# Kernel optimization log

Hardware: AMD Instinct MI355X
Metric: run time of the kernel (lower is better)

## Reference

```python
import jax, jax.numpy as jnp
import numpy as np

B, N, D, P, HMUL, K = 2, 4096, 64, 64, 4, 16
H = D * HMUL  # attn_mlp hidden = 256
EPS = 1e-5


def setup_inputs() -> dict:
    key = jax.random.key(0)
    ks = jax.random.split(key, 18)
    def lin(k, fan_in, shape):
        return (jax.random.normal(k, shape, dtype=jnp.float32) / np.sqrt(fan_in)).astype(jnp.float32)
    return {
        "x": jax.random.normal(ks[0], (B, N, D), dtype=jnp.float32),
        "pos": jax.random.uniform(ks[1], (B, N, 3), dtype=jnp.float32),
        "w_qkv": lin(ks[2], D, (D, 3 * D)), "b_qkv": jnp.zeros((3 * D,), jnp.float32),
        "w_p1": lin(ks[3], 3, (3, P)),     "b_p1": jnp.zeros((P,), jnp.float32),
        "w_p2": lin(ks[4], P, (P, D)),     "b_p2": jnp.zeros((D,), jnp.float32),
        "w_a1": lin(ks[5], D, (D, H)),     "b_a1": jnp.zeros((H,), jnp.float32),
        "w_a2": lin(ks[6], H, (H, D)),     "b_a2": jnp.zeros((D,), jnp.float32),
        "w_fc": lin(ks[7], D, (D, D)),     "b_fc": jnp.zeros((D,), jnp.float32),
        "gamma": jnp.ones((D,), jnp.float32), "beta": jnp.zeros((D,), jnp.float32),
    }


def reference(x, pos, w_qkv, b_qkv, w_p1, b_p1, w_p2, b_p2,
              w_a1, b_a1, w_a2, b_a2, w_fc, b_fc, gamma, beta):
    residual = x
    qkv = x @ w_qkv + b_qkv                      # [B,N,3D]
    q, k, v = jnp.split(qkv, 3, axis=-1)         # each [B,N,D]

    # full O(N^2) pairwise distances for KNN (smallest-k)
    rel = pos[:, :, None, :] - pos[:, None, :, :]       # [B,N,N,3]
    dist = jnp.sqrt(jnp.sum(rel * rel, axis=-1))        # [B,N,N]
    _, idx = jax.lax.top_k(-dist, K)                    # [B,N,K] nearest indices

    # gather neighbors (gather commutes with the pointwise MLPs the torch
    # code applies before its neighbor_select, so math is identical)
    gather = jax.vmap(lambda arr, i: arr[i])            # arr:[N,*], i:[N,K] -> [N,K,*]
    k_nb = gather(k, idx)                               # [B,N,K,D]
    v_nb = gather(v, idx)                               # [B,N,K,D]
    pos_nb = gather(pos, idx)                           # [B,N,K,3]

    qk_map = q[:, :, None, :] - k_nb                    # [B,N,K,D]
    rel_nb = pos[:, :, None, :] - pos_nb                # [B,N,K,3]
    pos_emb = jax.nn.relu(rel_nb @ w_p1 + b_p1) @ w_p2 + b_p2   # [B,N,K,D]

    h = qk_map + pos_emb
    scores = jax.nn.relu(h @ w_a1 + b_a1) @ w_a2 + b_a2          # [B,N,K,D]
    attn = jax.nn.softmax(scores, axis=-2)                       # over K neighbors
    agg = jnp.sum(attn * v_nb, axis=-2)                          # [B,N,D]

    agg = agg @ w_fc + b_fc
    # BatchNorm1d over channel dim D (training-mode batch stats over B and N)
    mean = jnp.mean(agg, axis=(0, 1))
    var = jnp.mean(jnp.square(agg - mean), axis=(0, 1))
    agg = (agg - mean) * jax.lax.rsqrt(var + EPS) * gamma + beta
    return jax.nn.relu(agg) + residual
```

## Files before the change

kernel.cpp:

```cpp
#include <hip/hip_runtime.h>
#include <hip/hip_bf16.h>
#include <math.h>

#define NPTS 4096
#define KNB 16
#define CAP 384
#define QPB 8

typedef __attribute__((ext_vector_type(8))) short bf16x8;
typedef __attribute__((ext_vector_type(4))) float f32x4;
#define MFMA16(a, b, c) __builtin_amdgcn_mfma_f32_16x16x32_bf16(a, b, c, 0, 0, 0)

__device__ __forceinline__ unsigned short f2bf(float f) {
  unsigned int u = __float_as_uint(f);
  unsigned int r = (u + 0x7fffu + ((u >> 16) & 1u)) >> 16;
  return (unsigned short)r;
}

__global__ __launch_bounds__(256) void qkv_pack_kernel(
    const float* __restrict__ x, const float* __restrict__ w_qkv,
    const float* __restrict__ b_qkv, float* __restrict__ qkv,
    const float* __restrict__ w_a1, const float* __restrict__ w_a2,
    const float* __restrict__ w_p2, unsigned short* __restrict__ pk1,
    unsigned short* __restrict__ pk2, unsigned short* __restrict__ pkp,
    float* __restrict__ stats) {
  int tid = threadIdx.x, bid = blockIdx.x;

  if (bid == 272) {
    if (tid < 128) stats[tid] = 0.f;
    return;
  }
  if (bid >= 128) {
    int e = (bid - 128) * 256 + tid;
    if (e < 16384) {
      int j = e & 7, lane = (e >> 3) & 63, t = e >> 9;
      int ks = t & 1, nt = t >> 1;
      int k = ks * 32 + ((lane >> 4) << 3) + j, n = nt * 16 + (lane & 15);
      pk1[e] = f2bf(w_a1[k * 256 + n]);
    } else if (e < 32768) {
      int e2 = e - 16384;
      int j = e2 & 7, lane = (e2 >> 3) & 63, t = e2 >> 9;
      int ks = t & 7, nt = t >> 3;
      int k = ks * 32 + ((lane >> 4) << 3) + j, n = nt * 16 + (lane & 15);
      pk2[e2] = f2bf(w_a2[k * 64 + n]);
    } else if (e < 36864) {
      int e3 = e - 32768;
      int j = e3 & 7, lane = (e3 >> 3) & 63, t = e3 >> 9;
      int ks = t & 1, nt = t >> 1;
      int k = ks * 32 + ((lane >> 4) << 3) + j, n = nt * 16 + (lane & 15);
      pkp[e3] = f2bf(w_p2[k * 64 + n]);
    }
    return;
  }

  int lane = tid & 63, w = tid >> 6;
  int m = lane & 15, quad = lane >> 4;
  int r0w = bid * 64 + w * 16;

  const float* xr = x + (size_t)(r0w + m) * 64;
  float xa[8], xb[8];
  *(float4*)&xa[0] = *(const float4*)(xr + quad * 8);
  *(float4*)&xa[4] = *(const float4*)(xr + quad * 8 + 4);
  *(float4*)&xb[0] = *(const float4*)(xr + 32 + quad * 8);
  *(float4*)&xb[4] = *(const float4*)(xr + 32 + quad * 8 + 4);
  bf16x8 a0, a1;
#pragma unroll
  for (int j = 0; j < 8; ++j) {
    a0[j] = (short)f2bf(xa[j]);
    a1[j] = (short)f2bf(xb[j]);
  }

#pragma unroll 4
  for (int nt = 0; nt < 12; ++nt) {
    int n = nt * 16 + m;
    int k0 = quad * 8;
    bf16x8 b0, b1;
#pragma unroll
    for (int j = 0; j < 8; ++j) {
      b0[j] = (short)f2bf(w_qkv[(size_t)(k0 + j) * 192 + n]);
      b1[j] = (short)f2bf(w_qkv[(size_t)(32 + k0 + j) * 192 + n]);
    }
    f32x4 acc = {0.f, 0.f, 0.f, 0.f};
    acc = MFMA16(a0, b0, acc);
    acc = MFMA16(a1, b1, acc);
    float bb = b_qkv[n];
#pragma unroll
    for (int i = 0; i < 4; ++i)
      qkv[(size_t)(r0w + quad * 4 + i) * 192 + n] = acc[i] + bb;
  }
}

__global__ __launch_bounds__(256, 4) void fused_kernel(
    const float* __restrict__ qkv, const float* __restrict__ pos,
    const unsigned short* __restrict__ pk1,
    const unsigned short* __restrict__ pk2,
    const unsigned short* __restrict__ pkp, const float* __restrict__ w_p1,
    const float* __restrict__ b_p1, const float* __restrict__ b_p2,
    const float* __restrict__ b_a1, const float* __restrict__ b_a2,
    const float* __restrict__ w_fc, const float* __restrict__ b_fc,
    float* __restrict__ y, float* __restrict__ stats) {
  __shared__ __align__(16) char smem[25216];
  __shared__ int s_idx[128];

  int tid = threadIdx.x, lane = tid & 63, w = tid >> 6;
  int m = lane & 15, quad = lane >> 4;
  int g0 = blockIdx.x * QPB;
  int b = g0 >> 12;
  const float* posb = pos + (size_t)b * NPTS * 3;

  {
    unsigned int(*cbits)[CAP] = (unsigned int(*)[CAP])smem;
    int(*cidx)[CAP] = (int(*)[CAP])(smem + 12288);
    unsigned long long* wmin = (unsigned long long*)(smem + 24576);
    float* sretry = (float*)(smem + 24608);
    unsigned int* scnt = (unsigned int*)(smem + 24640);
    unsigned long long* sprev = (unsigned long long*)(smem + 24672);
    int* sany = (int*)(smem + 24680);

    float qx[QPB], qy[QPB], qz[QPB];
#pragma unroll
    for (int q = 0; q < QPB; ++q) {
      int i = (g0 + q) & (NPTS - 1);
      qx[q] = posb[i * 3 + 0];
      qy[q] = posb[i * 3 + 1];
      qz[q] = posb[i * 3 + 2];
    }
    if (tid < QPB) scnt[tid] = 0;
    if (tid == 0) sany[0] = 0;
    __syncthreads();

    const float T2 = 0.015625f;
    for (int c = 0; c < NPTS / 256; ++c) {
      int j = c * 256 + tid;
      int j3 = j * 3;
      float px = posb[j3 + 0], py = posb[j3 + 1], pz = posb[j3 + 2];
#pragma unroll
      for (int q = 0; q < QPB; ++q) {
        float dx = qx[q] - px, dy = qy[q] - py, dz = qz[q] - pz;
        float d2 = fmaf(dz, dz, fmaf(dy, dy, dx * dx));
        bool hit = d2 < T2;
        unsigned long long mask = __ballot(hit);
        if (mask) {
          if (hit) {
            unsigned int p = atomicAdd(&scnt[q], 1u);
            if (p < CAP) {
              cbits[q][p] = __float_as_uint(d2);
              cidx[q][p] = j;
            }
          }
        }
      }
    }
    __syncthreads();

    if (tid < QPB) {
      int q = tid;
      unsigned int n = scnt[q];
      float nt = 0.f;
      if (n < KNB) nt = 0.0625f;
      else if (n > CAP) nt = 0.00390625f;
      sretry[q] = nt;
      if (nt != 0.f) {
        scnt[q] = 0;
        sany[0] = 1;
      }
    }
    __syncthreads();

    if (sany[0]) {
      float tr[QPB];
#pragma unroll
      for (int q = 0; q < QPB; ++q) tr[q] = sretry[q];
      for (int c = 0; c < NPTS / 256; ++c) {
        int j = c * 256 + tid;
        int j3 = j * 3;
        float px = posb[j3 + 0], py = posb[j3 + 1], pz = posb[j3 + 2];
#pragma unroll
        for (int q = 0; q < QPB; ++q) {
          if (tr[q] != 0.f) {
            float dx = qx[q] - px, dy = qy[q] - py, dz = qz[q] - pz;
            float d2 = fmaf(dz, dz, fmaf(dy, dy, dx * dx));
            bool hit = d2 < tr[q];
            unsigned long long mask = __ballot(hit);
            if (mask) {
              if (hit) {
                unsigned int p = atomicAdd(&scnt[q], 1u);
                if (p < CAP) {
                  cbits[q][p] = __float_as_uint(d2);
                  cidx[q][p] = j;
                }
              }
            }
          }
        }
      }
      __syncthreads();
    }

    for (int qq = 0; qq < 2; ++qq) {
      int q = w * 2 + qq;
      int L = (int)scnt[q];
      if (L >= KNB && L <= CAP) {
        for (int i = lane; i < L; i += 64) {
          unsigned long long ki = ((unsigned long long)cbits[q][i] << 32) |
                                  (unsigned int)cidx[q][i];
          int rank = 0;
          for (int mm = 0; mm < L; ++mm) {
            unsigned long long km = ((unsigned long long)cbits[q][mm] << 32) |
                                    (unsigned int)cidx[q][mm];
            rank += km < ki;
          }
          if (rank < KNB) s_idx[q * KNB + rank] = cidx[q][i];
        }
      }
    }
    __syncthreads();

    for (int q = 0; q < QPB; ++q) {
      unsigned int n = scnt[q];
      if (n < KNB || n > CAP) {
        unsigned long long prev = 0ull;
        for (int r = 0; r < KNB; ++r) {
          unsigned long long best = ~0ull;
          for (int c = 0; c < NPTS / 256; ++c) {
            int j = c * 256 + tid;
            float dx = qx[q] - posb[j * 3 + 0];
            float dy = qy[q] - posb[j * 3 + 1];
            float dz = qz[q] - posb[j * 3 + 2];
            float d2 = fmaf(dz, dz, fmaf(dy, dy, dx * dx));
            unsigned long long key =
                ((unsigned long long)__float_as_uint(d2) << 32) |
                (unsigned int)j;
            bool ok = (r == 0) || (key > prev);
            best = (ok && key < best) ? key : best;
          }
#pragma unroll
          for (int off = 32; off > 0; off >>= 1) {
            unsigned long long o = __shfl_down(best, off);
            best = best < o ? best : o;
          }
          if (lane == 0) wmin[w] = best;
          __syncthreads();
          if (tid == 0) {
            unsigned long long m0 = wmin[0], m1 = wmin[1];
            unsigned long long m2 = wmin[2], m3 = wmin[3];
            unsigned long long a = m0 < m1 ? m0 : m1;
            unsigned long long d = m2 < m3 ? m2 : m3;
            a = a < d ? a : d;
            s_idx[q * KNB + r] = (int)(unsigned int)a;
            sprev[0] = a;
          }
          __syncthreads();
          prev = sprev[0];
          __syncthreads();
        }
      }
    }
  }
  __syncthreads();

  unsigned short(*region)[72] = (unsigned short(*)[72])smem;
  float(*s_rel)[32][3] = (float(*)[32][3])(smem + 18432);

  if (lane < 32) {
    int row = 32 * w + lane;
    int p = lane >> 4;
    int g = g0 + 2 * w + p;
    int jb = (b << 12) | s_idx[row];
    s_rel[w][lane][0] = pos[(size_t)g * 3 + 0] - pos[(size_t)jb * 3 + 0];
    s_rel[w][lane][1] = pos[(size_t)g * 3 + 1] - pos[(size_t)jb * 3 + 1];
    s_rel[w][lane][2] = pos[(size_t)g * 3 + 2] - pos[(size_t)jb * 3 + 2];
  }

  {
    float w0 = w_p1[lane], w1 = w_p1[64 + lane], w2 = w_p1[128 + lane];
    float bp = b_p1[lane];
    for (int rl = 0; rl < 32; ++rl) {
      int row = 32 * w + rl;
      float rx = s_rel[w][rl][0], ry = s_rel[w][rl][1], rz = s_rel[w][rl][2];
      float e = fmaf(rz, w2, fmaf(ry, w1, fmaf(rx, w0, bp)));
      region[row][lane] = f2bf(fmaxf(e, 0.f));
    }
  }

  {
    bf16x8 ea0[2], ea1[2];
#pragma unroll
    for (int p = 0; p < 2; ++p) {
      ea0[p] = *(const bf16x8*)&region[32 * w + 16 * p + m][quad * 8];
      ea1[p] = *(const bf16x8*)&region[32 * w + 16 * p + m][32 + quad * 8];
    }
#pragma unroll
    for (int nt = 0; nt < 4; ++nt) {
      bf16x8 b0 = *(const bf16x8*)(pkp + ((size_t)(nt * 2 + 0) * 64 + lane) * 8);
      bf16x8 b1 = *(const bf16x8*)(pkp + ((size_t)(nt * 2 + 1) * 64 + lane) * 8);
      int col = nt * 16 + m;
      float bp2 = b_p2[col];
#pragma unroll
      for (int p = 0; p < 2; ++p) {
        f32x4 acc = {0.f, 0.f, 0.f, 0.f};
        acc = MFMA16(ea0[p], b0, acc);
        acc = MFMA16(ea1[p], b1, acc);
        int g = g0 + 2 * w + p;
        float qv = qkv[(size_t)g * 192 + col];
#pragma unroll
        for (int i = 0; i < 4; ++i) {
          int row = 32 * w + 16 * p + quad * 4 + i;
          int jb = (b << 12) | s_idx[row];
          float kv = qkv[(size_t)jb * 192 + 64 + col];
          region[row][col] = f2bf(qv - kv + acc[i] + bp2);
        }
      }
    }
  }

  float vreg[2][4][4];
#pragma unroll
  for (int p = 0; p < 2; ++p)
#pragma unroll
    for (int i = 0; i < 4; ++i) {
      int row = 32 * w + 16 * p + quad * 4 + i;
      int jb = (b << 12) | s_idx[row];
      const float* vr = qkv + (size_t)jb * 192 + 128;
#pragma unroll
      for (int nt2 = 0; nt2 < 4; ++nt2) vreg[p][nt2][i] = vr[nt2 * 16 + m];
    }

  bf16x8 ha0[2], ha1[2];
#pragma unroll
  for (int p = 0; p < 2; ++p) {
    ha0[p] = *(const bf16x8*)&region[32 * w + 16 * p + m][quad * 8];
    ha1[p] = *(const bf16x8*)&region[32 * w + 16 * p + m][32 + quad * 8];
  }
  f32x4 acc2[2][4];
#pragma unroll
  for (int p = 0; p < 2; ++p)
#pragma unroll
    for (int nt2 = 0; nt2 < 4; ++nt2) acc2[p][nt2] = (f32x4){0.f, 0.f, 0.f, 0.f};

  unsigned short(*s_tc)[72] = (unsigned short(*)[72])(smem + w * 4608);

#pragma unroll
  for (int c = 0; c < 4; ++c) {
#pragma unroll
    for (int ntc = 0; ntc < 4; ++ntc) {
      int nt = 4 * c + ntc;
      bf16x8 b0 = *(const bf16x8*)(pk1 + ((size_t)(nt * 2 + 0) * 64 + lane) * 8);
      bf16x8 b1 = *(const bf16x8*)(pk1 + ((size_t)(nt * 2 + 1) * 64 + lane) * 8);
      int coll = ntc * 16 + m;
      float ba = b_a1[nt * 16 + m];
#pragma unroll
      for (int p = 0; p < 2; ++p) {
        f32x4 t = {0.f, 0.f, 0.f, 0.f};
        t = MFMA16(ha0[p], b0, t);
        t = MFMA16(ha1[p], b1, t);
#pragma unroll
        for (int i = 0; i < 4; ++i)
          s_tc[16 * p + quad * 4 + i][coll] = f2bf(fmaxf(t[i] + ba, 0.f));
      }
    }
#pragma unroll
    for (int sub = 0; sub < 2; ++sub) {
      int ks = c * 2 + sub;
      bf16x8 a[2];
#pragma unroll
      for (int p = 0; p < 2; ++p)
        a[p] = *(const bf16x8*)&s_tc[16 * p + m][sub * 32 + quad * 8];
#pragma unroll
      for (int nt2 = 0; nt2 < 4; ++nt2) {
        bf16x8 bb =
            *(const bf16x8*)(pk2 + ((size_t)(nt2 * 8 + ks) * 64 + lane) * 8);
#pragma unroll
        for (int p = 0; p < 2; ++p) acc2[p][nt2] = MFMA16(a[p], bb, acc2[p][nt2]);
      }
    }
  }

  float ba2[4];
#pragma unroll
  for (int nt2 = 0; nt2 < 4; ++nt2) ba2[nt2] = b_a2[nt2 * 16 + m];
  float aggv[2][4];
#pragma unroll
  for (int p = 0; p < 2; ++p) {
#pragma unroll
    for (int nt2 = 0; nt2 < 4; ++nt2) {
      float sc[4];
#pragma unroll
      for (int i = 0; i < 4; ++i) sc[i] = acc2[p][nt2][i] + ba2[nt2];
      float mx = fmaxf(fmaxf(sc[0], sc[1]), fmaxf(sc[2], sc[3]));
      mx = fmaxf(mx, __shfl_xor(mx, 16));
      mx = fmaxf(mx, __shfl_xor(mx, 32));
      float ex[4], ss = 0.f;
#pragma unroll
      for (int i = 0; i < 4; ++i) {
        ex[i] = exp2f((sc[i] - mx) * 1.4426950408889634f);
        ss += ex[i];
      }
      ss += __shfl_xor(ss, 16);
      ss += __shfl_xor(ss, 32);
      float nu = 0.f;
#pragma unroll
      for (int i = 0; i < 4; ++i) nu = fmaf(ex[i], vreg[p][nt2][i], nu);
      nu += __shfl_xor(nu, 16);
      nu += __shfl_xor(nu, 32);
      aggv[p][nt2] = nu / ss;
    }
  }
  __syncthreads();

  float* s_agg = (float*)smem;
  if (quad == 0) {
#pragma unroll
    for (int p = 0; p < 2; ++p)
#pragma unroll
      for (int nt2 = 0; nt2 < 4; ++nt2)
        s_agg[(2 * w + p) * 64 + nt2 * 16 + m] = aggv[p][nt2];
  }
  __syncthreads();

  {
    int c = lane, r = w;
    float acc0 = b_fc[c], acc1 = b_fc[c];
    for (int d = 0; d < 64; ++d) {
      float wv = w_fc[d * 64 + c];
      acc0 = fmaf(s_agg[r * 64 + d], wv, acc0);
      acc1 = fmaf(s_agg[(r + 4) * 64 + d], wv, acc1);
    }
    y[(size_t)(g0 + r) * 64 + c] = acc0;
    y[(size_t)(g0 + r + 4) * 64 + c] = acc1;
    float* s_red = (float*)(smem + 2048);
    float* s_red2 = (float*)(smem + 3072);
    s_red[w * 64 + c] = acc0 + acc1;
    s_red2[w * 64 + c] = acc0 * acc0 + acc1 * acc1;
  }
  __syncthreads();
  if (tid < 64) {
    float* s_red = (float*)(smem + 2048);
    float* s_red2 = (float*)(smem + 3072);
    float s = s_red[tid] + s_red[64 + tid] + s_red[128 + tid] + s_red[192 + tid];
    float s2 =
        s_red2[tid] + s_red2[64 + tid] + s_red2[128 + tid] + s_red2[192 + tid];
    atomicAdd(&stats[tid], s);
    atomicAdd(&stats[64 + tid], s2);
  }
}

__global__ __launch_bounds__(256) void bn_kernel(
    const float* __restrict__ y, const float* __restrict__ x,
    const float* __restrict__ stats, const float* __restrict__ gamma,
    const float* __restrict__ beta, float* __restrict__ out) {
  size_t o = (size_t)blockIdx.x * 256 + threadIdx.x;
  int c = (int)(o & 63);
  const float inv_n = 1.f / 8192.f;
  float mean = stats[c] * inv_n;
  float var = stats[64 + c] * inv_n - mean * mean;
  float inv = rsqrtf(var + 1e-5f);
  float v = (y[o] - mean) * inv * gamma[c] + beta[c];
  out[o] = fmaxf(v, 0.f) + x[o];
}

extern "C" void kernel_launch(void* const* d_in, const int* in_sizes, int n_in,
                              void* d_out, int out_size, void* d_ws,
                              size_t ws_size, hipStream_t stream) {
  const float* x = (const float*)d_in[0];
  const float* pos = (const float*)d_in[1];
  const float* w_qkv = (const float*)d_in[2];
  const float* b_qkv = (const float*)d_in[3];
  const float* w_p1 = (const float*)d_in[4];
  const float* b_p1 = (const float*)d_in[5];
  const float* w_p2 = (const float*)d_in[6];
  const float* b_p2 = (const float*)d_in[7];
  const float* w_a1 = (const float*)d_in[8];
  const float* b_a1 = (const float*)d_in[9];
  const float* w_a2 = (const float*)d_in[10];
  const float* b_a2 = (const float*)d_in[11];
  const float* w_fc = (const float*)d_in[12];
  const float* b_fc = (const float*)d_in[13];
  const float* gamma = (const float*)d_in[14];
  const float* beta = (const float*)d_in[15];

  char* ws = (char*)d_ws;
  float* qkv = (float*)(ws + 0);
  float* y = (float*)(ws + 8912896);
  float* stats = (float*)(ws + 11010048);
  unsigned short* pk1 = (unsigned short*)(ws + 11010560);
  unsigned short* pk2 = (unsigned short*)(ws + 11043328);
  unsigned short* pkp = (unsigned short*)(ws + 11076096);

  hipLaunchKernelGGL(qkv_pack_kernel, dim3(273), dim3(256), 0, stream, x,
                     w_qkv, b_qkv, qkv, w_a1, w_a2, w_p2, pk1, pk2, pkp,
                     stats);
  hipLaunchKernelGGL(fused_kernel, dim3(1024), dim3(256), 0, stream, qkv, pos,
                     pk1, pk2, pkp, w_p1, b_p1, b_p2, b_a1, b_a2, w_fc, b_fc,
                     y, stats);
  hipLaunchKernelGGL(bn_kernel, dim3(2048), dim3(256), 0, stream, y, x, stats,
                     gamma, beta, (float*)d_out);
}
```

Before: 148.7 us.

## Bucket points into a uniform spatial grid for KNN candidate search

```diff
diff --git a/kernel.cpp b/kernel.cpp
--- a/kernel.cpp
+++ b/kernel.cpp
@@ -15,6 +15,10 @@
   unsigned int u = __float_as_uint(f);
   unsigned int r = (u + 0x7fffu + ((u >> 16) & 1u)) >> 16;
   return (unsigned short)r;
+}
+__device__ __forceinline__ int cell1d(float v) {
+  int c = (int)(v * 8.f);
+  return c < 0 ? 0 : (c > 7 ? 7 : c);
 }
 
 __global__ __launch_bounds__(256) void qkv_pack_kernel(
@@ -23,11 +27,48 @@
     const float* __restrict__ w_a1, const float* __restrict__ w_a2,
     const float* __restrict__ w_p2, unsigned short* __restrict__ pk1,
     unsigned short* __restrict__ pk2, unsigned short* __restrict__ pkp,
-    float* __restrict__ stats) {
+    const float* __restrict__ pos, float4* __restrict__ spos,
+    unsigned int* __restrict__ gstart, float* __restrict__ stats) {
+  __shared__ unsigned int gcnt[512];
+  __shared__ unsigned int gst[513];
   int tid = threadIdx.x, bid = blockIdx.x;
 
-  if (bid == 272) {
+  if (bid == 274) {
     if (tid < 128) stats[tid] = 0.f;
+    return;
+  }
+  if (bid >= 272) {
+    int b = bid - 272;
+    const float* posb = pos + (size_t)b * NPTS * 3;
+    for (int i = tid; i < 512; i += 256) gcnt[i] = 0;
+    __syncthreads();
+    for (int i = tid; i < NPTS; i += 256) {
+      int cx = cell1d(posb[i * 3 + 0]);
+      int cy = cell1d(posb[i * 3 + 1]);
+      int cz = cell1d(posb[i * 3 + 2]);
+      atomicAdd(&gcnt[(cx * 8 + cy) * 8 + cz], 1u);
+    }
+    __syncthreads();
+    if (tid == 0) {
+      unsigned int s = 0;
+      for (int c = 0; c < 512; ++c) {
+        gst[c] = s;
+        s += gcnt[c];
+      }
+      gst[512] = s;
+    }
+    __syncthreads();
+    for (int i = tid; i < 513; i += 256) gstart[b * 513 + i] = gst[i];
+    for (int i = tid; i < 512; i += 256) gcnt[i] = 0;
+    __syncthreads();
+    for (int i = tid; i < NPTS; i += 256) {
+      float px = posb[i * 3 + 0], py = posb[i * 3 + 1], pz = posb[i * 3 + 2];
+      int cell = (cell1d(px) * 8 + cell1d(py)) * 8 + cell1d(pz);
+      unsigned int p = atomicAdd(&gcnt[cell], 1u);
+      float4 v;
+      v.x = px; v.y = py; v.z = pz; v.w = __int_as_float(i);
+      spos[(size_t)b * NPTS + gst[cell] + p] = v;
+    }
     return;
   }
   if (bid >= 128) {
@@ -92,6 +133,7 @@
 
 __global__ __launch_bounds__(256, 4) void fused_kernel(
     const float* __restrict__ qkv, const float* __restrict__ pos,
+    const float4* __restrict__ spos, const unsigned int* __restrict__ gstart,
     const unsigned short* __restrict__ pk1,
     const unsigned short* __restrict__ pk2,
     const unsigned short* __restrict__ pkp, const float* __restrict__ w_p1,
@@ -107,15 +149,15 @@
   int g0 = blockIdx.x * QPB;
   int b = g0 >> 12;
   const float* posb = pos + (size_t)b * NPTS * 3;
+  const float4* sposb = spos + (size_t)b * NPTS;
+  const unsigned int* gsb = gstart + b * 513;
 
   {
     unsigned int(*cbits)[CAP] = (unsigned int(*)[CAP])smem;
     int(*cidx)[CAP] = (int(*)[CAP])(smem + 12288);
     unsigned long long* wmin = (unsigned long long*)(smem + 24576);
-    float* sretry = (float*)(smem + 24608);
-    unsigned int* scnt = (unsigned int*)(smem + 24640);
-    unsigned long long* sprev = (unsigned long long*)(smem + 24672);
-    int* sany = (int*)(smem + 24680);
+    unsigned int* scnt = (unsigned int*)(smem + 24608);
+    unsigned long long* sprev = (unsigned long long*)(smem + 24640);
 
     float qx[QPB], qy[QPB], qz[QPB];
 #pragma unroll
@@ -125,80 +167,52 @@
       qy[q] = posb[i * 3 + 1];
       qz[q] = posb[i * 3 + 2];
     }
-    if (tid < QPB) scnt[tid] = 0;
-    if (tid == 0) sany[0] = 0;
-    __syncthreads();
-
-    const float T2 = 0.015625f;
-    for (int c = 0; c < NPTS / 256; ++c) {
-      int j = c * 256 + tid;
-      int j3 = j * 3;
-      float px = posb[j3 + 0], py = posb[j3 + 1], pz = posb[j3 + 2];
-#pragma unroll
-      for (int q = 0; q < QPB; ++q) {
-        float dx = qx[q] - px, dy = qy[q] - py, dz = qz[q] - pz;
-        float d2 = fmaf(dz, dz, fmaf(dy, dy, dx * dx));
-        bool hit = d2 < T2;
-        unsigned long long mask = __ballot(hit);
-        if (mask) {
-          if (hit) {
-            unsigned int p = atomicAdd(&scnt[q], 1u);
-            if (p < CAP) {
-              cbits[q][p] = __float_as_uint(d2);
-              cidx[q][p] = j;
-            }
-          }
-        }
-      }
-    }
-    __syncthreads();
-
-    if (tid < QPB) {
-      int q = tid;
-      unsigned int n = scnt[q];
-      float nt = 0.f;
-      if (n < KNB) nt = 0.0625f;
-      else if (n > CAP) nt = 0.00390625f;
-      sretry[q] = nt;
-      if (nt != 0.f) {
-        scnt[q] = 0;
-        sany[0] = 1;
-      }
-    }
-    __syncthreads();
-
-    if (sany[0]) {
-      float tr[QPB];
-#pragma unroll
-      for (int q = 0; q < QPB; ++q) tr[q] = sretry[q];
-      for (int c = 0; c < NPTS / 256; ++c) {
-        int j = c * 256 + tid;
-        int j3 = j * 3;
-        float px = posb[j3 + 0], py = posb[j3 + 1], pz = posb[j3 + 2];
-#pragma unroll
-        for (int q = 0; q < QPB; ++q) {
-          if (tr[q] != 0.f) {
-            float dx = qx[q] - px, dy = qy[q] - py, dz = qz[q] - pz;
-            float d2 = fmaf(dz, dz, fmaf(dy, dy, dx * dx));
-            bool hit = d2 < tr[q];
-            unsigned long long mask = __ballot(hit);
-            if (mask) {
-              if (hit) {
-                unsigned int p = atomicAdd(&scnt[q], 1u);
-                if (p < CAP) {
-                  cbits[q][p] = __float_as_uint(d2);
-                  cidx[q][p] = j;
+    if (lane == 0) {
+      scnt[2 * w] = 0;
+      scnt[2 * w + 1] = 0;
+    }
+
+    for (int qq = 0; qq < 2; ++qq) {
+      int q = 2 * w + qq;
+      float qxx = qx[q], qyy = qy[q], qzz = qz[q];
+      int cx = cell1d(qxx), cy = cell1d(qyy), cz = cell1d(qzz);
+      float T = 0.015625f;
+      int R = 1;
+      for (int attempt = 0; attempt < 2; ++attempt) {
+        int x0 = cx - R < 0 ? 0 : cx - R, x1 = cx + R > 7 ? 7 : cx + R;
+        int y0 = cy - R < 0 ? 0 : cy - R, y1 = cy + R > 7 ? 7 : cy + R;
+        int z0 = cz - R < 0 ? 0 : cz - R, z1 = cz + R > 7 ? 7 : cz + R;
+        for (int xx = x0; xx <= x1; ++xx) {
+          for (int yy = y0; yy <= y1; ++yy) {
+            int rowc = (xx * 8 + yy) * 8;
+            unsigned int s = gsb[rowc + z0];
+            unsigned int e = gsb[rowc + z1 + 1];
+            for (unsigned int i = s + lane; i < e; i += 64) {
+              float4 p = sposb[i];
+              float dx = qxx - p.x, dy = qyy - p.y, dz = qzz - p.z;
+              float d2 = fmaf(dz, dz, fmaf(dy, dy, dx * dx));
+              if (d2 < T) {
+                unsigned int pp = atomicAdd(&scnt[q], 1u);
+                if (pp < CAP) {
+                  cbits[q][pp] = __float_as_uint(d2);
+                  cidx[q][pp] = __float_as_int(p.w);
                 }
               }
             }
           }
         }
-      }
-      __syncthreads();
+        if (attempt == 0 && scnt[q] < KNB) {
+          if (lane == 0) scnt[q] = 0;
+          T = 0.0625f;
+          R = 2;
+        } else {
+          break;
+        }
+      }
     }
 
     for (int qq = 0; qq < 2; ++qq) {
-      int q = w * 2 + qq;
+      int q = 2 * w + qq;
       int L = (int)scnt[q];
       if (L >= KNB && L <= CAP) {
         for (int i = lane; i < L; i += 64) {
@@ -481,18 +495,20 @@
 
   char* ws = (char*)d_ws;
   float* qkv = (float*)(ws + 0);
+  float4* spos = (float4*)(ws + 6291456);
+  unsigned int* gstart = (unsigned int*)(ws + 6422528);
   float* y = (float*)(ws + 8912896);
   float* stats = (float*)(ws + 11010048);
   unsigned short* pk1 = (unsigned short*)(ws + 11010560);
   unsigned short* pk2 = (unsigned short*)(ws + 11043328);
   unsigned short* pkp = (unsigned short*)(ws + 11076096);
 
-  hipLaunchKernelGGL(qkv_pack_kernel, dim3(273), dim3(256), 0, stream, x,
-                     w_qkv, b_qkv, qkv, w_a1, w_a2, w_p2, pk1, pk2, pkp,
-                     stats);
+  hipLaunchKernelGGL(qkv_pack_kernel, dim3(275), dim3(256), 0, stream, x,
+                     w_qkv, b_qkv, qkv, w_a1, w_a2, w_p2, pk1, pk2, pkp, pos,
+                     spos, gstart, stats);
   hipLaunchKernelGGL(fused_kernel, dim3(1024), dim3(256), 0, stream, qkv, pos,
-                     pk1, pk2, pkp, w_p1, b_p1, b_p2, b_a1, b_a2, w_fc, b_fc,
-                     y, stats);
+                     spos, gstart, pk1, pk2, pkp, w_p1, b_p1, b_p2, b_a1, b_a2,
+                     w_fc, b_fc, y, stats);
   hipLaunchKernelGGL(bn_kernel, dim3(2048), dim3(256), 0, stream, y, x, stats,
                      gamma, beta, (float*)d_out);
 }
```

New measurement: 165.3 us. 11.1% more time.
